# Kernel tuning notes

Hardware: AMD Instinct MI355X
Metric: run time of the kernel (lower is better)

The kernel has to match this reference:

```python
import jax, jax.numpy as jnp
import numpy as np

B, T, C = 1, 2048, 1024
H = 16
HD = C // H  # 64
K = 8
EPS = 1e-6
NEG = -1.0e9


def apply_rotary_emb(x, cos, sin):
    # x: (B,T,H,HD), cos/sin: (T, HD//2)
    x1, x2 = jnp.split(x, 2, axis=-1)
    c = cos[None, :, None, :]
    s = sin[None, :, None, :]
    return jnp.concatenate([x1 * c - x2 * s, x1 * s + x2 * c], axis=-1)


def rms_norm(x):
    return x * jax.lax.rsqrt(jnp.mean(jnp.square(x), axis=-1, keepdims=True) + EPS)


def setup_inputs() -> dict:
    key = jax.random.key(0)
    ks = jax.random.split(key, 8)
    x = jax.random.normal(ks[0], (B, T, C), dtype=jnp.float32)
    # standard RoPE tables
    inv_freq = 1.0 / (10000.0 ** (np.arange(0, HD, 2, dtype=np.float32) / HD))
    t = np.arange(T, dtype=np.float32)
    freqs = np.outer(t, inv_freq)  # (T, HD//2)
    cos = jnp.asarray(np.cos(freqs), dtype=jnp.float32)
    sin = jnp.asarray(np.sin(freqs), dtype=jnp.float32)
    std = 0.02
    Wq = std * jax.random.normal(ks[1], (C, C), dtype=jnp.float32)
    Wk = std * jax.random.normal(ks[2], (C, C), dtype=jnp.float32)
    Wv = std * jax.random.normal(ks[3], (C, C), dtype=jnp.float32)
    Wproj = std * jax.random.normal(ks[4], (C, C), dtype=jnp.float32)
    Wdq = jax.random.normal(ks[5], (C, K), dtype=jnp.float32) / np.sqrt(C)
    Wdk = jax.random.normal(ks[6], (C, K), dtype=jnp.float32) / np.sqrt(C)
    return {"x": x, "cos": cos, "sin": sin, "Wq": Wq, "Wk": Wk, "Wv": Wv,
            "Wproj": Wproj, "Wdq": Wdq, "Wdk": Wdk}


def reference(x, cos, sin, Wq, Wk, Wv, Wproj, Wdq, Wdk):
    b, t, c = x.shape
    q = (x @ Wq).reshape(b, t, H, HD)
    k = (x @ Wk).reshape(b, t, H, HD)
    v = (x @ Wv).reshape(b, t, H, HD)
    q = rms_norm(apply_rotary_emb(q, cos, sin))
    k = rms_norm(apply_rotary_emb(k, cos, sin))

    # digit projections (identical for every head in the source module)
    qd = x @ Wdq  # (B,T,K)
    kd = x @ Wdk  # (B,T,K)
    matches = qd[:, :, None, :] == kd[:, None, :, :]  # (B,Tq,Tk,K)
    prefix = jnp.cumprod(matches.astype(jnp.int32), axis=-1)
    lcp = jnp.sum(prefix, axis=-1)  # (B,Tq,Tk)
    lcp_mask = lcp >= (K - 1)

    causal = jnp.tril(jnp.ones((t, t), dtype=bool))
    combined = causal[None, None, :, :] & lcp_mask[:, None, :, :]  # (B,1->H,Tq,Tk)

    scale = 1.0 / jnp.sqrt(jnp.asarray(HD, x.dtype))
    scores = jnp.einsum('bqhd,bkhd->bhqk', q * scale, k)
    scores = jnp.where(combined, scores, NEG)
    w = jax.nn.softmax(scores, axis=-1)
    y = jnp.einsum('bhqk,bkhd->bqhd', w, v).reshape(b, t, c)
    return y @ Wproj
```

## Files before the change

### kernel.cpp

```cpp
#include <hip/hip_runtime.h>
#include <math.h>

#define T_DIM 2048
#define C_DIM 1024
#define H_NUM 16
#define HD_DIM 64
#define K_LCP 8
#define NEG_VAL -1.0e9f
#define NBLK 256

typedef __bf16 bf16;
typedef __bf16 bf16x4 __attribute__((ext_vector_type(4)));
typedef __bf16 bf16x8 __attribute__((ext_vector_type(8)));
typedef float f32x4 __attribute__((ext_vector_type(4)));
typedef unsigned long long u64;

#define ALOAD(p) __hip_atomic_load((p), __ATOMIC_RELAXED, __HIP_MEMORY_SCOPE_AGENT)
#define ASTORE(p, v) \
  __hip_atomic_store((p), (v), __ATOMIC_RELAXED, __HIP_MEMORY_SCOPE_AGENT)

__device__ __forceinline__ u64 pk2(float lo, float hi) {
  return (u64)__float_as_uint(lo) | ((u64)__float_as_uint(hi) << 32);
}
__device__ __forceinline__ float upk_lo(u64 u) {
  return __uint_as_float((unsigned)u);
}
__device__ __forceinline__ float upk_hi(u64 u) {
  return __uint_as_float((unsigned)(u >> 32));
}

struct Prm {
  const float *x, *cosT, *sinT, *Wq, *Wk, *Wv, *Wproj, *Wdq, *Wdk;
  float* out;
  bf16 *xb, *wqt, *wkt, *wvt, *wpt, *qB, *kB, *vB;
  float *qd, *kd, *vtsum, *partial;
  int *tilemask, *allmask;
  u64* maskbits;
  float *vmean, *rowout;
  int* flags;
  int* bars;
};

__device__ __forceinline__ void gbar(int* bars, int slot, bool fence) {
  __syncthreads();
  if (threadIdx.x == 0) {
    if (fence) __threadfence();
    int* B = bars + slot * 32;
    const int g = blockIdx.x >> 5;
    int old = __hip_atomic_fetch_add(&B[1 + g], 1, __ATOMIC_RELAXED,
                                     __HIP_MEMORY_SCOPE_AGENT);
    if (old == 31) {
      __hip_atomic_fetch_add(&B[0], 1, __ATOMIC_RELAXED,
                             __HIP_MEMORY_SCOPE_AGENT);
      while (__hip_atomic_load(&B[0], __ATOMIC_RELAXED,
                               __HIP_MEMORY_SCOPE_AGENT) < 8)
        __builtin_amdgcn_s_sleep(8);
      ASTORE(&B[10 + g], 1);
    } else {
      while (ALOAD(&B[10 + g]) == 0) __builtin_amdgcn_s_sleep(2);
    }
    if (fence) __threadfence();
  }
  __syncthreads();
}

template <int TMt, int MI, int NA>
__device__ void gemm_body(bf16* As, bf16* Bs, const bf16* A, const bf16* Bt,
                          void* Cv, int bx, int by, int z, int mode,
                          const float* cosT, const float* sinT, float* vtsum) {
  const int tid = threadIdx.x;
  const int Kd = C_DIM, N = C_DIM;
  const int bm = by * TMt;
  const int bn = bx * 128;
  const int wave = tid >> 6, lane = tid & 63;
  const int lr = lane >> 2;
  const int lc = (lane & 3) * 8;
  bf16* gA = (bf16*)(A + (size_t)(bm + wave * 16 * NA + lr) * Kd + lc);
  bf16* gB = (bf16*)(Bt + (size_t)(bn + wave * 32 + lr) * Kd + lc);
  bf16* lA = As + wave * 512 * NA;
  bf16* lB = Bs + wave * 1024;
  const int wr = (wave >> 1) * (MI * 16);
  const int wc = (wave & 1) * 64;
  const int fm = lane & 15;
  const int fk_ = (lane >> 4) * 8;

  f32x4 acc[MI][4] = {};
  for (int k0 = 0; k0 < Kd; k0 += 32) {
    __syncthreads();
#pragma unroll
    for (int u = 0; u < NA; ++u)
      __builtin_amdgcn_global_load_lds(
          (__attribute__((address_space(1))) void*)(gA + (size_t)u * 16 * Kd + k0),
          (__attribute__((address_space(3))) void*)(lA + u * 512), 16, 0, 0);
#pragma unroll
    for (int u = 0; u < 2; ++u)
      __builtin_amdgcn_global_load_lds(
          (__attribute__((address_space(1))) void*)(gB + (size_t)u * 16 * Kd + k0),
          (__attribute__((address_space(3))) void*)(lB + u * 512), 16, 0, 0);
    __syncthreads();
    bf16x8 af[MI], bfr[4];
#pragma unroll
    for (int i = 0; i < MI; ++i)
      af[i] = *(const bf16x8*)(As + (size_t)(wr + i * 16 + fm) * 32 + fk_);
#pragma unroll
    for (int j = 0; j < 4; ++j)
      bfr[j] = *(const bf16x8*)(Bs + (size_t)(wc + j * 16 + fm) * 32 + fk_);
#pragma unroll
    for (int i = 0; i < MI; ++i)
#pragma unroll
      for (int j = 0; j < 4; ++j)
        acc[i][j] = __builtin_amdgcn_mfma_f32_16x16x32_bf16(af[i], bfr[j],
                                                            acc[i][j], 0, 0, 0);
  }
  const int cq = (lane >> 4) * 4;
  if (mode && z < 2) {
    bf16* C = (bf16*)Cv;
#pragma unroll
    for (int i = 0; i < MI; ++i)
#pragma unroll
      for (int r = 0; r < 4; ++r) {
        const int t = bm + wr + i * 16 + cq + r;
        float c0 = cosT[(size_t)t * 32 + fm], s0 = sinT[(size_t)t * 32 + fm];
        float c1 = cosT[(size_t)t * 32 + 16 + fm];
        float s1 = sinT[(size_t)t * 32 + 16 + fm];
        float a0 = acc[i][0][r], a1 = acc[i][1][r];
        float a2 = acc[i][2][r], a3 = acc[i][3][r];
        float o0 = a0 * c0 - a2 * s0, o2 = a0 * s0 + a2 * c0;
        float o1 = a1 * c1 - a3 * s1, o3 = a1 * s1 + a3 * c1;
        float ss = o0 * o0 + o1 * o1 + o2 * o2 + o3 * o3;
        ss += __shfl_xor(ss, 1);
        ss += __shfl_xor(ss, 2);
        ss += __shfl_xor(ss, 4);
        ss += __shfl_xor(ss, 8);
        float rn = 1.0f / sqrtf(ss * (1.0f / 64.0f) + 1e-6f);
        size_t base = (size_t)t * N + bn + wc + fm;
        C[base + 0] = (bf16)(o0 * rn);
        C[base + 16] = (bf16)(o1 * rn);
        C[base + 32] = (bf16)(o2 * rn);
        C[base + 48] = (bf16)(o3 * rn);
      }
  } else if (mode) {
    bf16* C = (bf16*)Cv;
#pragma unroll
    for (int i = 0; i < MI; ++i)
#pragma unroll
      for (int r = 0; r < 4; ++r) {
        size_t base = (size_t)(bm + wr + i * 16 + cq + r) * N + bn + wc + fm;
#pragma unroll
        for (int j = 0; j < 4; ++j) C[base + j * 16] = (bf16)acc[i][j][r];
      }
    const int kt = (bm + wr) >> 6;
#pragma unroll
    for (int j = 0; j < 4; ++j) {
      float s = 0.f;
#pragma unroll
      for (int i = 0; i < MI; ++i)
#pragma unroll
        for (int r = 0; r < 4; ++r) s += acc[i][j][r];
      s += __shfl_xor(s, 16);
      s += __shfl_xor(s, 32);
      if ((lane >> 4) == 0)
        vtsum[(size_t)kt * C_DIM + bn + wc + j * 16 + fm] = s;
    }
  } else {
    float* C = (float*)Cv;
#pragma unroll
    for (int i = 0; i < MI; ++i)
#pragma unroll
      for (int r = 0; r < 4; ++r) {
        size_t base = (size_t)(bm + wr + i * 16 + cq + r) * N + bn + wc + fm;
#pragma unroll
        for (int j = 0; j < 4; ++j) C[base + j * 16] = acc[i][j][r];
      }
  }
}

__device__ inline void write_vmean16(const float* vmp, bf16* yp) {
  f32x4 a0 = ((const f32x4*)vmp)[0];
  f32x4 a1 = ((const f32x4*)vmp)[1];
  f32x4 a2 = ((const f32x4*)vmp)[2];
  f32x4 a3 = ((const f32x4*)vmp)[3];
  bf16x8 o0 = {(bf16)a0[0], (bf16)a0[1], (bf16)a0[2], (bf16)a0[3],
               (bf16)a1[0], (bf16)a1[1], (bf16)a1[2], (bf16)a1[3]};
  bf16x8 o1 = {(bf16)a2[0], (bf16)a2[1], (bf16)a2[2], (bf16)a2[3],
               (bf16)a3[0], (bf16)a3[1], (bf16)a3[2], (bf16)a3[3]};
  *(bf16x8*)yp = o0;
  *(bf16x8*)(yp + 8) = o1;
}

__device__ void attn_body(int q64, int h, const bf16* q, const bf16* k,
                          const bf16* v, const float* vtsum,
                          const float* vmean, const u64* maskbits,
                          const int* tilemask, const int* allmask,
                          const int* pneed, bf16* y, char* smem) {
  bf16 (*vsT)[72] = (bf16(*)[72])smem;
  bf16 (*ps)[16][72] = (bf16(*)[16][72])(smem + 9216);
  int (*tmS)[32] = (int(*)[32])(smem + 18432);
  const int q0 = q64 * 64;
  const int tid = threadIdx.x;
  const int wv = tid >> 6;
  const int lane = tid & 63;
  const int qb0 = q0 >> 4;

  const int a0 = allmask[qb0 + 0], a1 = allmask[qb0 + 1];
  const int a2 = allmask[qb0 + 2], a3 = allmask[qb0 + 3];
  const int pn = pneed[q0 >> 6];
  if (a0 & a1 & a2 & a3) {
    if (pn) {
      const int row = tid >> 2, d0 = (tid & 3) * 16;
      write_vmean16(vmean + h * HD_DIM + d0,
                    y + (size_t)(q0 + row) * C_DIM + h * HD_DIM + d0);
    }
    return;
  }
  const int w_active = !((wv == 0) ? a0 : (wv == 1) ? a1 : (wv == 2) ? a2 : a3);

  if (tid < 128)
    tmS[tid >> 5][tid & 31] = tilemask[(size_t)(qb0 + (tid >> 5)) * 32 + (tid & 31)];

  if (!w_active && pn) {
    const int row = wv * 16 + (lane >> 2), d0 = (lane & 3) * 16;
    write_vmean16(vmean + h * HD_DIM + d0,
                  y + (size_t)(q0 + row) * C_DIM + h * HD_DIM + d0);
  }

  const int fm = lane & 15;
  const int fk = (lane >> 4) * 8;
  bf16x8 aq0 = {}, aq1 = {};
  if (w_active) {
    const bf16* qp = q + (size_t)(q0 + wv * 16 + fm) * C_DIM + h * HD_DIM;
    aq0 = *(const bf16x8*)(qp + fk);
    aq1 = *(const bf16x8*)(qp + 32 + fk);
  }
  __syncthreads();

  float m[4] = {-INFINITY, -INFINITY, -INFINITY, -INFINITY};
  float l[4] = {0.f, 0.f, 0.f, 0.f};
  f32x4 out[4] = {};

  for (int kt = 0; kt < T_DIM / 64; ++kt) {
    const int need = tmS[0][kt] | tmS[1][kt] | tmS[2][kt] | tmS[3][kt];
    const int k0 = kt * 64;
    if (need) {
      __syncthreads();
      {
        const int row = tid & 63, d0 = (tid >> 6) * 16;
        const bf16* vp = v + (size_t)(k0 + row) * C_DIM + h * HD_DIM + d0;
        bf16x8 v0 = *(const bf16x8*)(vp);
        bf16x8 v1 = *(const bf16x8*)(vp + 8);
#pragma unroll
        for (int i = 0; i < 8; ++i) vsT[d0 + i][row] = v0[i];
#pragma unroll
        for (int i = 0; i < 8; ++i) vsT[d0 + 8 + i][row] = v1[i];
      }
      __syncthreads();
    }
    if (!w_active) continue;
    if (tmS[wv][kt]) {
      u64 mwr[4];
#pragma unroll
      for (int r = 0; r < 4; ++r)
        mwr[r] = maskbits[(size_t)(q0 + wv * 16 + (lane >> 4) * 4 + r) * 32 + kt] >> fm;
      f32x4 s[4] = {};
#pragma unroll
      for (int j = 0; j < 4; ++j) {
        const bf16* kp = k + (size_t)(k0 + j * 16 + fm) * C_DIM + h * HD_DIM;
        bf16x8 bk0 = *(const bf16x8*)(kp + fk);
        bf16x8 bk1 = *(const bf16x8*)(kp + 32 + fk);
        s[j] = __builtin_amdgcn_mfma_f32_16x16x32_bf16(aq0, bk0, s[j], 0, 0, 0);
        s[j] = __builtin_amdgcn_mfma_f32_16x16x32_bf16(aq1, bk1, s[j], 0, 0, 0);
      }
      float xv[4][4];
      float tmax[4] = {NEG_VAL, NEG_VAL, NEG_VAL, NEG_VAL};
#pragma unroll
      for (int j = 0; j < 4; ++j)
#pragma unroll
        for (int r = 0; r < 4; ++r) {
          float val = ((mwr[r] >> (16 * j)) & 1ull) ? s[j][r] * 0.125f : NEG_VAL;
          xv[j][r] = val;
          tmax[r] = fmaxf(tmax[r], val);
        }
#pragma unroll
      for (int r = 0; r < 4; ++r) {
#pragma unroll
        for (int off = 1; off < 16; off <<= 1)
          tmax[r] = fmaxf(tmax[r], __shfl_xor(tmax[r], off));
      }
      float alpha[4], lsum[4] = {0.f, 0.f, 0.f, 0.f};
#pragma unroll
      for (int r = 0; r < 4; ++r) {
        float mn = fmaxf(m[r], tmax[r]);
        alpha[r] = __expf(m[r] - mn);
        m[r] = mn;
      }
#pragma unroll
      for (int j = 0; j < 4; ++j)
#pragma unroll
        for (int r = 0; r < 4; ++r) {
          float pp = __expf(xv[j][r] - m[r]);
          lsum[r] += pp;
          ps[wv][(lane >> 4) * 4 + r][j * 16 + fm] = (bf16)pp;
        }
#pragma unroll
      for (int r = 0; r < 4; ++r) {
#pragma unroll
        for (int off = 1; off < 16; off <<= 1) lsum[r] += __shfl_xor(lsum[r], off);
        l[r] = l[r] * alpha[r] + lsum[r];
      }
#pragma unroll
      for (int jd = 0; jd < 4; ++jd)
#pragma unroll
        for (int r = 0; r < 4; ++r) out[jd][r] *= alpha[r];
      bf16x8 pa0 = *(const bf16x8*)&ps[wv][fm][fk];
      bf16x8 pa1 = *(const bf16x8*)&ps[wv][fm][32 + fk];
#pragma unroll
      for (int jd = 0; jd < 4; ++jd) {
        bf16x8 bv0 = *(const bf16x8*)&vsT[jd * 16 + fm][fk];
        bf16x8 bv1 = *(const bf16x8*)&vsT[jd * 16 + fm][32 + fk];
        out[jd] = __builtin_amdgcn_mfma_f32_16x16x32_bf16(pa0, bv0, out[jd], 0, 0, 0);
        out[jd] = __builtin_amdgcn_mfma_f32_16x16x32_bf16(pa1, bv1, out[jd], 0, 0, 0);
      }
    } else {
      int needu = (m[0] <= NEG_VAL) | (m[1] <= NEG_VAL) | (m[2] <= NEG_VAL) |
                  (m[3] <= NEG_VAL);
      if (needu) {
#pragma unroll
        for (int jd = 0; jd < 4; ++jd) {
          float vt = vtsum[(size_t)kt * C_DIM + h * HD_DIM + jd * 16 + fm];
#pragma unroll
          for (int r = 0; r < 4; ++r)
            if (m[r] <= NEG_VAL) out[jd][r] += vt;
        }
#pragma unroll
        for (int r = 0; r < 4; ++r)
          if (m[r] <= NEG_VAL) {
            m[r] = NEG_VAL;
            l[r] += 64.f;
          }
      }
    }
  }

  if (w_active) {
#pragma unroll
    for (int r = 0; r < 4; ++r) {
      float inv_l = 1.0f / l[r];
      bf16* yp = y + (size_t)(q0 + wv * 16 + (lane >> 4) * 4 + r) * C_DIM +
                 h * HD_DIM + fm;
#pragma unroll
      for (int jd = 0; jd < 4; ++jd) yp[jd * 16] = (bf16)(out[jd][r] * inv_l);
    }
  }
}

__global__ __launch_bounds__(256, 2) void mono(Prm p) {
  const int gid = blockIdx.x;
  const int tid = threadIdx.x;
  const int wave = tid >> 6, lane = tid & 63;
  __shared__ __align__(16) char smem[19456];

  int* qneed = p.flags;
  int* kneed = p.flags + 16;
  int* vneed = p.flags + 32;
  int* pneed = p.flags + 48;
  int* anyfl = p.flags + 80;

  for (int rr = 0; rr < 2; ++rr) {
    const int t = gid * 8 + rr * 4 + wave;
    const float* xp = p.x + (size_t)t * C_DIM;
    float aq[8] = {}, ak[8] = {};
#pragma unroll
    for (int i = 0; i < 16; ++i) {
      const int c = i * 64 + lane;
      float xv = xp[c];
      float4 wq0 = *(const float4*)(p.Wdq + (size_t)c * K_LCP);
      float4 wq1 = *(const float4*)(p.Wdq + (size_t)c * K_LCP + 4);
      float4 wk0 = *(const float4*)(p.Wdk + (size_t)c * K_LCP);
      float4 wk1 = *(const float4*)(p.Wdk + (size_t)c * K_LCP + 4);
      aq[0] = fmaf(xv, wq0.x, aq[0]); aq[1] = fmaf(xv, wq0.y, aq[1]);
      aq[2] = fmaf(xv, wq0.z, aq[2]); aq[3] = fmaf(xv, wq0.w, aq[3]);
      aq[4] = fmaf(xv, wq1.x, aq[4]); aq[5] = fmaf(xv, wq1.y, aq[5]);
      aq[6] = fmaf(xv, wq1.z, aq[6]); aq[7] = fmaf(xv, wq1.w, aq[7]);
      ak[0] = fmaf(xv, wk0.x, ak[0]); ak[1] = fmaf(xv, wk0.y, ak[1]);
      ak[2] = fmaf(xv, wk0.z, ak[2]); ak[3] = fmaf(xv, wk0.w, ak[3]);
      ak[4] = fmaf(xv, wk1.x, ak[4]); ak[5] = fmaf(xv, wk1.y, ak[5]);
      ak[6] = fmaf(xv, wk1.z, ak[6]); ak[7] = fmaf(xv, wk1.w, ak[7]);
    }
#pragma unroll
    for (int j = 0; j < 8; ++j) {
#pragma unroll
      for (int off = 32; off >= 1; off >>= 1) {
        aq[j] += __shfl_xor(aq[j], off);
        ak[j] += __shfl_xor(ak[j], off);
      }
    }
    if (lane == 0) {
      u64* qdp = (u64*)(p.qd + (size_t)t * K_LCP);
      u64* kdp = (u64*)(p.kd + (size_t)t * K_LCP);
#pragma unroll
      for (int j = 0; j < 4; ++j) {
        ASTORE(qdp + j, pk2(aq[2 * j], aq[2 * j + 1]));
        ASTORE(kdp + j, pk2(ak[2 * j], ak[2 * j + 1]));
      }
    }
  }
  if (gid < 32) {
    f32x4 s = {0.f, 0.f, 0.f, 0.f};
    for (int r = 0; r < 64; ++r)
      s += ((const f32x4*)(p.x + (size_t)(gid * 64 + r) * C_DIM))[tid];
    u64* dst = (u64*)(p.partial + (size_t)gid * C_DIM) + tid * 2;
    ASTORE(dst + 0, pk2(s[0], s[1]));
    ASTORE(dst + 1, pk2(s[2], s[3]));
  } else {
    const int jbp = (gid & 15) * 64;
    float accp = 0.f;
#pragma unroll
    for (int k = 0; k < 16; ++k)
      accp += p.Wproj[(size_t)((tid >> 2) + k * 64) * C_DIM + jbp + (tid & 3) * 16];
    asm volatile("" ::"v"(accp));
    if (gid >= 128 && gid < 192) {
      const int b = gid - 128, cs = (b >> 4) * 256, jbv = (b & 15) * 64;
      float accv = 0.f;
#pragma unroll
      for (int k = 0; k < 4; ++k)
        accv += p.Wv[(size_t)(cs + (tid >> 2) + k * 64) * C_DIM + jbv + (tid & 3) * 16];
      asm volatile("" ::"v"(accv));
    }
  }
  gbar(p.bars, 0, false);

  if (gid < 128) {
    const int qb = gid;
    float (*qds)[K_LCP] = (float(*)[K_LCP])smem;
    int* tm = (int*)(smem + 512);
    if (tid < 32) tm[tid] = 0;
    if (tid < 64) {
      u64 u = ALOAD((u64*)(p.qd + (size_t)qb * 16 * K_LCP) + tid);
      qds[tid >> 2][(tid & 3) * 2 + 0] = upk_lo(u);
      qds[tid >> 2][(tid & 3) * 2 + 1] = upk_hi(u);
    }
    __syncthreads();
    const int nit = (qb >> 4) + 1;
    for (int it = 0; it < nit; ++it) {
      const int key = it * 256 + wave * 64 + lane;
      const u64* kp = (const u64*)(p.kd + (size_t)key * K_LCP);
      float kv[K_LCP];
#pragma unroll
      for (int jj = 0; jj < 4; ++jj) {
        u64 u = ALOAD(kp + jj);
        kv[2 * jj + 0] = upk_lo(u);
        kv[2 * jj + 1] = upk_hi(u);
      }
      const int grp = it * 4 + wave;
      u64 anyb = 0ull;
#pragma unroll
      for (int ql = 0; ql < 16; ++ql) {
        const int qg = qb * 16 + ql;
        bool pr = (key <= qg) & (qds[ql][0] == kv[0]) & (qds[ql][1] == kv[1]) &
                  (qds[ql][2] == kv[2]) & (qds[ql][3] == kv[3]) &
                  (qds[ql][4] == kv[4]) & (qds[ql][5] == kv[5]) &
                  (qds[ql][6] == kv[6]);
        u64 b = __ballot(pr);
        anyb |= b;
        if (lane == 0) ASTORE(p.maskbits + (size_t)qg * 32 + grp, b);
      }
      if (lane == 0 && anyb) tm[grp] = 1;
    }
    __syncthreads();
    int anytm = 0;
#pragma unroll
    for (int i = 0; i < 32; ++i) anytm |= tm[i];
    if (tid < 32) ASTORE(p.tilemask + qb * 32 + tid, tm[tid]);
    if (tid == 0) ASTORE(p.allmask + qb, !anytm);
    if (anytm) {
      if (tid < 32) {
        if (tm[tid]) atomicOr(&kneed[tid >> 1], 1);
        atomicOr(&vneed[tid >> 1], 1);
      }
      if (tid == 0) {
        atomicOr(&qneed[qb >> 3], 1);
        atomicOr(&pneed[qb >> 2], 1);
        atomicOr(anyfl, 1);
      }
    }
  } else if (gid < 192) {
    const int b = gid - 128;
    const int cs = (b >> 4) * 256;
    const int jb = (b & 15) * 64;
    float* xm = (float*)smem;
    f32x4 (*xr)[64] = (f32x4(*)[64])(smem + 1024);
    f32x4 (*red)[16] = (f32x4(*)[16])(smem + 5120);
    const int pg = tid >> 6, t6 = tid & 63;
    {
      f32x4 s = {0.f, 0.f, 0.f, 0.f};
      for (int g = pg * 8; g < pg * 8 + 8; ++g) {
        const u64* pp = (const u64*)(p.partial + (size_t)g * C_DIM + cs) + t6 * 2;
        u64 a = ALOAD(pp + 0), bu = ALOAD(pp + 1);
        s[0] += upk_lo(a); s[1] += upk_hi(a);
        s[2] += upk_lo(bu); s[3] += upk_hi(bu);
      }
      xr[pg][t6] = s;
      __syncthreads();
      if (pg == 0) {
        f32x4 t = (xr[0][t6] + xr[1][t6]) + (xr[2][t6] + xr[3][t6]);
        t *= (1.0f / 2048.0f);
        *(f32x4*)&xm[t6 * 4] = t;
      }
      __syncthreads();
    }
    const int jg = tid & 15, pq = tid >> 4;
    f32x4 acc = {0.f, 0.f, 0.f, 0.f};
#pragma unroll 4
    for (int i = 0; i < 16; ++i) {
      const int c = pq * 16 + i;
      acc += xm[c] * *(const f32x4*)(p.Wv + (size_t)(cs + c) * C_DIM + jb + jg * 4);
    }
    red[pq][jg] = acc;
    __syncthreads();
    if (tid < 64) {
      float s = 0.f;
#pragma unroll
      for (int q = 0; q < 16; ++q) s += red[q][tid >> 2][tid & 3];
      atomicAdd(&p.vmean[jb + tid], s);
    }
  }
  gbar(p.bars, 1, false);

  __shared__ int anyS;
  if (tid == 0) anyS = ALOAD(anyfl);
  __syncthreads();
  const int any = anyS;

  if (!any) {
    float* xm = (float*)smem;
    f32x4 (*red)[16] = (f32x4(*)[16])(smem + 4096);
    float* rs = (float*)(smem + 8192);
#pragma unroll
    for (int kk = 0; kk < 4; ++kk)
      xm[tid * 4 + kk] = ALOAD(p.vmean + tid * 4 + kk);
    __syncthreads();
    const int jb = (gid & 15) * 64;
    const int jg = tid & 15, pq = tid >> 4;
    f32x4 acc = {0.f, 0.f, 0.f, 0.f};
#pragma unroll 8
    for (int i = 0; i < 64; ++i) {
      const int c = pq * 64 + i;
      acc += xm[c] * *(const f32x4*)(p.Wproj + (size_t)c * C_DIM + jb + jg * 4);
    }
    red[pq][jg] = acc;
    __syncthreads();
    if (tid < 64) {
      float s = 0.f;
#pragma unroll
      for (int q = 0; q < 16; ++q) s += red[q][tid >> 2][tid & 3];
      rs[tid] = s;
    }
    __syncthreads();
    const int r0 = (gid >> 4) * 128;
    f32x4 v4 = *(const f32x4*)&rs[(tid & 15) * 4];
#pragma unroll
    for (int kk = 0; kk < 8; ++kk) {
      const int row = r0 + (tid >> 4) + kk * 16;
      *(f32x4*)(p.out + (size_t)row * C_DIM + jb + (tid & 15) * 4) = v4;
    }
    return;
  }

  if (tid == 0) __threadfence();
  __syncthreads();
  for (int rr = 0; rr < 8; ++rr) {
    const int t = gid * 8 + rr;
    float4 f = *(const float4*)(p.x + (size_t)t * C_DIM + tid * 4);
    bf16x4 o = {(bf16)f.x, (bf16)f.y, (bf16)f.z, (bf16)f.w};
    *(bf16x4*)(p.xb + (size_t)t * C_DIM + tid * 4) = o;
  }
  {
    bf16 (*tile)[67] = (bf16(*)[67])smem;
    for (int it = 0; it < 4; ++it) {
      const int idx = gid * 4 + it;
      const int z = idx >> 8;
      const float* W = (z == 0) ? p.Wq : (z == 1) ? p.Wk : (z == 2) ? p.Wv : p.Wproj;
      bf16* O = (z == 0) ? p.wqt : (z == 1) ? p.wkt : (z == 2) ? p.wvt : p.wpt;
      const int rem = idx & 255;
      const int bk = (rem >> 4) * 64;
      const int bn = (rem & 15) * 64;
      __syncthreads();
      {
        const int r = tid >> 2;
        const int c0 = (tid & 3) * 16;
        const float* src = W + (size_t)(bk + r) * C_DIM + bn + c0;
#pragma unroll
        for (int t = 0; t < 16; t += 4) {
          float4 f = *(const float4*)(src + t);
          tile[r][c0 + t + 0] = (bf16)f.x;
          tile[r][c0 + t + 1] = (bf16)f.y;
          tile[r][c0 + t + 2] = (bf16)f.z;
          tile[r][c0 + t + 3] = (bf16)f.w;
        }
      }
      __syncthreads();
      {
        const int n = tid >> 2;
        const int k0 = (tid & 3) * 16;
        bf16x8 lo, hi;
#pragma unroll
        for (int j = 0; j < 8; ++j) lo[j] = tile[k0 + j][n];
#pragma unroll
        for (int j = 0; j < 8; ++j) hi[j] = tile[k0 + 8 + j][n];
        bf16* dst = O + (size_t)(bn + n) * C_DIM + bk + k0;
        *(bf16x8*)dst = lo;
        *(bf16x8*)(dst + 8) = hi;
      }
    }
  }
  if (gid < 64) {
    __syncthreads();
    float* xm = (float*)smem;
    float (*red)[64] = (float(*)[64])(smem + 1024);
    const int cs = (gid >> 4) * 256;
    const int jb = (gid & 15) * 64;
    const int pq = tid >> 6, t6 = tid & 63;
    xm[tid] = ALOAD(p.vmean + cs + tid);
    __syncthreads();
    const int j = jb + t6;
    float acc = 0.f;
    for (int c = pq * 64; c < pq * 64 + 64; ++c)
      acc = fmaf(xm[c], p.Wproj[(size_t)(cs + c) * C_DIM + j], acc);
    red[pq][t6] = acc;
    __syncthreads();
    if (tid < 64)
      atomicAdd(&p.rowout[jb + tid],
                (red[0][tid] + red[1][tid]) + (red[2][tid] + red[3][tid]));
  }
  gbar(p.bars, 3, true);

  {
    bf16* As = (bf16*)smem;
    bf16* Bs = (bf16*)(smem + 8192);
    for (int v = gid; v < 384; v += 256) {
      __syncthreads();
      const int z = v >> 7, r = v & 127, by = r >> 3, bx = r & 7;
      const int* f = (z == 0) ? qneed : (z == 1) ? kneed : vneed;
      if (!f[by]) continue;
      const bf16* Bt = (z == 0) ? p.wqt : (z == 1) ? p.wkt : p.wvt;
      void* C = (z == 0) ? (void*)p.qB : (z == 1) ? (void*)p.kB : (void*)p.vB;
      gemm_body<128, 4, 2>(As, Bs, p.xb, Bt, C, bx, by, z, 1, p.cosT, p.sinT,
                           p.vtsum);
    }
  }
  gbar(p.bars, 4, true);

  for (int v = gid; v < 512; v += 256) {
    __syncthreads();
    attn_body(v & 31, v >> 5, p.qB, p.kB, p.vB, p.vtsum, p.vmean, p.maskbits,
              p.tilemask, p.allmask, pneed, p.xb , smem);
  }
  gbar(p.bars, 5, true);

  {
    bf16* As = (bf16*)smem;
    bf16* Bs = (bf16*)(smem + 8192);
    const int by = gid >> 3, bx = gid & 7;
    if (pneed[by])
      gemm_body<64, 2, 1>(As, Bs, p.xb , p.wpt, (void*)p.out, bx, by, 2,
                          0, p.cosT, p.sinT, nullptr);
    f32x4 v4;
    v4[0] = ALOAD(p.rowout + tid * 4 + 0);
    v4[1] = ALOAD(p.rowout + tid * 4 + 1);
    v4[2] = ALOAD(p.rowout + tid * 4 + 2);
    v4[3] = ALOAD(p.rowout + tid * 4 + 3);
#pragma unroll
    for (int r = 0; r < 8; ++r) {
      const int row = gid * 8 + r;
      if (!pneed[row >> 6])
        ((f32x4*)(p.out + (size_t)row * C_DIM))[tid] = v4;
    }
  }
}

extern "C" void kernel_launch(void* const* d_in, const int* in_sizes, int n_in,
                              void* d_out, int out_size, void* d_ws, size_t ws_size,
                              hipStream_t stream) {
  char* ws = (char*)d_ws;
  const size_t TC2 = (size_t)T_DIM * C_DIM * 2;
  const size_t CC2 = (size_t)C_DIM * C_DIM * 2;
  Prm p;
  p.x = (const float*)d_in[0];
  p.cosT = (const float*)d_in[1];
  p.sinT = (const float*)d_in[2];
  p.Wq = (const float*)d_in[3];
  p.Wk = (const float*)d_in[4];
  p.Wv = (const float*)d_in[5];
  p.Wproj = (const float*)d_in[6];
  p.Wdq = (const float*)d_in[7];
  p.Wdk = (const float*)d_in[8];
  p.out = (float*)d_out;
  p.xb = (bf16*)(ws + 0);
  p.wqt = (bf16*)(ws + TC2);
  p.wkt = (bf16*)(ws + TC2 + CC2);
  p.wvt = (bf16*)(ws + TC2 + 2 * CC2);
  p.wpt = (bf16*)(ws + TC2 + 3 * CC2);
  p.qB = (bf16*)(ws + TC2 + 4 * CC2);
  p.kB = (bf16*)(ws + 2 * TC2 + 4 * CC2);
  p.vB = (bf16*)(ws + 3 * TC2 + 4 * CC2);
  char* p2 = ws + 4 * TC2 + 4 * CC2;
  p.qd = (float*)p2;      p2 += (size_t)T_DIM * K_LCP * 4;
  p.kd = (float*)p2;      p2 += (size_t)T_DIM * K_LCP * 4;
  p.vtsum = (float*)p2;   p2 += 32 * C_DIM * 4;
  p.partial = (float*)p2; p2 += 32 * C_DIM * 4;
  p.tilemask = (int*)p2;  p2 += (T_DIM / 16) * 32 * 4;
  p.allmask = (int*)p2;   p2 += (T_DIM / 16) * 4;
  p.maskbits = (u64*)p2;  p2 += (size_t)T_DIM * 32 * 8;
  char* ctrl = p2;
  p.vmean = (float*)p2;   p2 += C_DIM * 4;
  p.rowout = (float*)p2;  p2 += C_DIM * 4;
  p.flags = (int*)p2;     p2 += 128 * 4;
  p.bars = (int*)p2;      p2 += 6 * 32 * 4;
  const size_t ctrl_bytes = (size_t)(p2 - ctrl);

  hipMemsetAsync(ctrl, 0, ctrl_bytes, stream);
  mono<<<NBLK, 256, 0, stream>>>(p);
}
```

Baseline: 137.5 us.

## Split persistent mono kernel into three launches at the first two grid barriers

The single persistent kernel is split into k1, k2 and k3 at its first two software grid barriers, so kernel launch boundaries replace the spin-wait barriers. With ordering now guaranteed by the launches, the relaxed atomic loads and stores of packed u64 values become plain vectorized float4 loads and stores, and some loops are unrolled. This removes the barrier spin and atomic traffic but adds two kernel launch gaps. Per-block work between the phases is otherwise unchanged.

```diff
diff --git a/kernel.cpp b/kernel.cpp
--- a/kernel.cpp
+++ b/kernel.cpp
@@ -18,16 +18,6 @@
 #define ALOAD(p) __hip_atomic_load((p), __ATOMIC_RELAXED, __HIP_MEMORY_SCOPE_AGENT)
 #define ASTORE(p, v) \
   __hip_atomic_store((p), (v), __ATOMIC_RELAXED, __HIP_MEMORY_SCOPE_AGENT)
-
-__device__ __forceinline__ u64 pk2(float lo, float hi) {
-  return (u64)__float_as_uint(lo) | ((u64)__float_as_uint(hi) << 32);
-}
-__device__ __forceinline__ float upk_lo(u64 u) {
-  return __uint_as_float((unsigned)u);
-}
-__device__ __forceinline__ float upk_hi(u64 u) {
-  return __uint_as_float((unsigned)(u >> 32));
-}
 
 struct Prm {
   const float *x, *cosT, *sinT, *Wq, *Wk, *Wv, *Wproj, *Wdq, *Wdk;
@@ -353,17 +343,10 @@
   }
 }
 
-__global__ __launch_bounds__(256, 2) void mono(Prm p) {
+__global__ __launch_bounds__(256, 2) void k1(Prm p) {
   const int gid = blockIdx.x;
   const int tid = threadIdx.x;
   const int wave = tid >> 6, lane = tid & 63;
-  __shared__ __align__(16) char smem[19456];
-
-  int* qneed = p.flags;
-  int* kneed = p.flags + 16;
-  int* vneed = p.flags + 32;
-  int* pneed = p.flags + 48;
-  int* anyfl = p.flags + 80;
 
   for (int rr = 0; rr < 2; ++rr) {
     const int t = gid * 8 + rr * 4 + wave;
@@ -395,22 +378,18 @@
       }
     }
     if (lane == 0) {
-      u64* qdp = (u64*)(p.qd + (size_t)t * K_LCP);
-      u64* kdp = (u64*)(p.kd + (size_t)t * K_LCP);
-#pragma unroll
-      for (int j = 0; j < 4; ++j) {
-        ASTORE(qdp + j, pk2(aq[2 * j], aq[2 * j + 1]));
-        ASTORE(kdp + j, pk2(ak[2 * j], ak[2 * j + 1]));
-      }
+      *(float4*)(p.qd + (size_t)t * K_LCP) = make_float4(aq[0], aq[1], aq[2], aq[3]);
+      *(float4*)(p.qd + (size_t)t * K_LCP + 4) = make_float4(aq[4], aq[5], aq[6], aq[7]);
+      *(float4*)(p.kd + (size_t)t * K_LCP) = make_float4(ak[0], ak[1], ak[2], ak[3]);
+      *(float4*)(p.kd + (size_t)t * K_LCP + 4) = make_float4(ak[4], ak[5], ak[6], ak[7]);
     }
   }
   if (gid < 32) {
     f32x4 s = {0.f, 0.f, 0.f, 0.f};
+#pragma unroll 8
     for (int r = 0; r < 64; ++r)
       s += ((const f32x4*)(p.x + (size_t)(gid * 64 + r) * C_DIM))[tid];
-    u64* dst = (u64*)(p.partial + (size_t)gid * C_DIM) + tid * 2;
-    ASTORE(dst + 0, pk2(s[0], s[1]));
-    ASTORE(dst + 1, pk2(s[2], s[3]));
+    ((f32x4*)(p.partial + (size_t)gid * C_DIM))[tid] = s;
   } else {
     const int jbp = (gid & 15) * 64;
     float accp = 0.f;
@@ -427,30 +406,34 @@
       asm volatile("" ::"v"(accv));
     }
   }
-  gbar(p.bars, 0, false);
+}
+
+__global__ __launch_bounds__(256, 2) void k2(Prm p) {
+  const int gid = blockIdx.x;
+  const int tid = threadIdx.x;
+  const int wave = tid >> 6, lane = tid & 63;
+  __shared__ __align__(16) char smem[9216];
+
+  int* qneed = p.flags;
+  int* kneed = p.flags + 16;
+  int* vneed = p.flags + 32;
+  int* pneed = p.flags + 48;
+  int* anyfl = p.flags + 80;
 
   if (gid < 128) {
     const int qb = gid;
     float (*qds)[K_LCP] = (float(*)[K_LCP])smem;
     int* tm = (int*)(smem + 512);
     if (tid < 32) tm[tid] = 0;
-    if (tid < 64) {
-      u64 u = ALOAD((u64*)(p.qd + (size_t)qb * 16 * K_LCP) + tid);
-      qds[tid >> 2][(tid & 3) * 2 + 0] = upk_lo(u);
-      qds[tid >> 2][(tid & 3) * 2 + 1] = upk_hi(u);
-    }
+    if (tid < 32)
+      ((float4*)qds)[tid] = ((const float4*)(p.qd + (size_t)qb * 16 * K_LCP))[tid];
     __syncthreads();
     const int nit = (qb >> 4) + 1;
     for (int it = 0; it < nit; ++it) {
       const int key = it * 256 + wave * 64 + lane;
-      const u64* kp = (const u64*)(p.kd + (size_t)key * K_LCP);
       float kv[K_LCP];
-#pragma unroll
-      for (int jj = 0; jj < 4; ++jj) {
-        u64 u = ALOAD(kp + jj);
-        kv[2 * jj + 0] = upk_lo(u);
-        kv[2 * jj + 1] = upk_hi(u);
-      }
+      *(float4*)&kv[0] = *(const float4*)(p.kd + (size_t)key * K_LCP);
+      *(float4*)&kv[4] = *(const float4*)(p.kd + (size_t)key * K_LCP + 4);
       const int grp = it * 4 + wave;
       u64 anyb = 0ull;
 #pragma unroll
@@ -462,7 +445,7 @@
                   (qds[ql][6] == kv[6]);
         u64 b = __ballot(pr);
         anyb |= b;
-        if (lane == 0) ASTORE(p.maskbits + (size_t)qg * 32 + grp, b);
+        if (lane == 0) p.maskbits[(size_t)qg * 32 + grp] = b;
       }
       if (lane == 0 && anyb) tm[grp] = 1;
     }
@@ -470,8 +453,8 @@
     int anytm = 0;
 #pragma unroll
     for (int i = 0; i < 32; ++i) anytm |= tm[i];
-    if (tid < 32) ASTORE(p.tilemask + qb * 32 + tid, tm[tid]);
-    if (tid == 0) ASTORE(p.allmask + qb, !anytm);
+    if (tid < 32) p.tilemask[qb * 32 + tid] = tm[tid];
+    if (tid == 0) p.allmask[qb] = !anytm;
     if (anytm) {
       if (tid < 32) {
         if (tm[tid]) atomicOr(&kneed[tid >> 1], 1);
@@ -483,7 +466,7 @@
         atomicOr(anyfl, 1);
       }
     }
-  } else if (gid < 192) {
+  } else {
     const int b = gid - 128;
     const int cs = (b >> 4) * 256;
     const int jb = (b & 15) * 64;
@@ -493,12 +476,9 @@
     const int pg = tid >> 6, t6 = tid & 63;
     {
       f32x4 s = {0.f, 0.f, 0.f, 0.f};
-      for (int g = pg * 8; g < pg * 8 + 8; ++g) {
-        const u64* pp = (const u64*)(p.partial + (size_t)g * C_DIM + cs) + t6 * 2;
-        u64 a = ALOAD(pp + 0), bu = ALOAD(pp + 1);
-        s[0] += upk_lo(a); s[1] += upk_hi(a);
-        s[2] += upk_lo(bu); s[3] += upk_hi(bu);
-      }
+#pragma unroll
+      for (int g = pg * 8; g < pg * 8 + 8; ++g)
+        s += ((const f32x4*)(p.partial + (size_t)g * C_DIM + cs))[t6];
       xr[pg][t6] = s;
       __syncthreads();
       if (pg == 0) {
@@ -524,10 +504,20 @@
       atomicAdd(&p.vmean[jb + tid], s);
     }
   }
-  gbar(p.bars, 1, false);
+}
+
+__global__ __launch_bounds__(256, 2) void k3(Prm p) {
+  const int gid = blockIdx.x;
+  const int tid = threadIdx.x;
+  __shared__ __align__(16) char smem[19456];
+
+  int* qneed = p.flags;
+  int* kneed = p.flags + 16;
+  int* vneed = p.flags + 32;
+  int* pneed = p.flags + 48;
 
   __shared__ int anyS;
-  if (tid == 0) anyS = ALOAD(anyfl);
+  if (tid == 0) anyS = p.flags[80];
   __syncthreads();
   const int any = anyS;
 
@@ -535,9 +525,7 @@
     float* xm = (float*)smem;
     f32x4 (*red)[16] = (f32x4(*)[16])(smem + 4096);
     float* rs = (float*)(smem + 8192);
-#pragma unroll
-    for (int kk = 0; kk < 4; ++kk)
-      xm[tid * 4 + kk] = ALOAD(p.vmean + tid * 4 + kk);
+    ((f32x4*)xm)[tid] = ((const f32x4*)p.vmean)[tid];
     __syncthreads();
     const int jb = (gid & 15) * 64;
     const int jg = tid & 15, pq = tid >> 4;
@@ -566,8 +554,6 @@
     return;
   }
 
-  if (tid == 0) __threadfence();
-  __syncthreads();
   for (int rr = 0; rr < 8; ++rr) {
     const int t = gid * 8 + rr;
     float4 f = *(const float4*)(p.x + (size_t)t * C_DIM + tid * 4);
@@ -620,7 +606,7 @@
     const int cs = (gid >> 4) * 256;
     const int jb = (gid & 15) * 64;
     const int pq = tid >> 6, t6 = tid & 63;
-    xm[tid] = ALOAD(p.vmean + cs + tid);
+    xm[tid] = p.vmean[cs + tid];
     __syncthreads();
     const int j = jb + t6;
     float acc = 0.f;
@@ -719,5 +705,7 @@
   const size_t ctrl_bytes = (size_t)(p2 - ctrl);
 
   hipMemsetAsync(ctrl, 0, ctrl_bytes, stream);
-  mono<<<NBLK, 256, 0, stream>>>(p);
+  k1<<<256, 256, 0, stream>>>(p);
+  k2<<<192, 256, 0, stream>>>(p);
+  k3<<<256, 256, 0, stream>>>(p);
 }
```

Result: faster. 119.4 us (-13.1%).
